# Optimization experiments

Measured on AMD Instinct MI355X. Metric: run time of the kernel, lower is better.

The kernel has to match this reference:

```python
import jax, jax.numpy as jnp
import numpy as np

B, S, D = 2, 2048, 1024
H, DH, DL = 16, 64, 512
E, DFF, K = 8, 2048, 2
EPS = 1e-5


def setup_inputs() -> dict:
    key = jax.random.key(0)
    ks = jax.random.split(key, 10)
    std = 0.02
    inp = {
        'x': jax.random.normal(ks[0], (B, S, D), jnp.float32),
        'mask': jnp.tril(jnp.ones((S, S), dtype=bool))[None, None],  # causal (1,1,S,S)
        'ln1_scale': jnp.ones((D,), jnp.float32),
        'ln1_bias': jnp.zeros((D,), jnp.float32),
        'Wq': jax.random.normal(ks[1], (D, H * DH), jnp.float32) * std,
        'Wdkv': jax.random.normal(ks[2], (D, DL), jnp.float32) * std,
        'Wukv': jax.random.normal(ks[3], (DL, H * DH), jnp.float32) * std,
        'Wo': jax.random.normal(ks[4], (H * DH, D), jnp.float32) * std,
        'ln2_scale': jnp.ones((D,), jnp.float32),
        'ln2_bias': jnp.zeros((D,), jnp.float32),
        'Wgate': jax.random.normal(ks[5], (D, E), jnp.float32) * std,
        'bgate': jnp.zeros((E,), jnp.float32),
        'We1': jax.random.normal(ks[6], (E, D, DFF), jnp.float32) * std,
        'be1': jnp.zeros((E, DFF), jnp.float32),
        'We2': jax.random.normal(ks[7], (E, DFF, D), jnp.float32) * std,
        'be2': jnp.zeros((E, D), jnp.float32),
    }
    return inp


def _layernorm(x, g, b):
    m = jnp.mean(x, axis=-1, keepdims=True)
    v = jnp.mean(jnp.square(x - m), axis=-1, keepdims=True)
    return (x - m) * jax.lax.rsqrt(v + EPS) * g + b


def reference(x, mask, ln1_scale, ln1_bias, Wq, Wdkv, Wukv, Wo,
              ln2_scale, ln2_bias, Wgate, bgate, We1, be1, We2, be2):
    b, s, d = x.shape
    # --- MLA attention ---
    h = _layernorm(x, ln1_scale, ln1_bias)
    q = (h @ Wq).reshape(b, s, H, DH)
    kv = ((h @ Wdkv) @ Wukv).reshape(b, s, H, DH)  # k == v == kv
    scores = jnp.einsum('bqhd,bkhd->bhqk', q, kv) / (DH ** 0.5)
    scores = jnp.where(mask, scores, -jnp.inf)
    probs = jax.nn.softmax(scores, axis=-1)
    attn = jnp.einsum('bhqk,bkhd->bqhd', probs, kv).reshape(b, s, H * DH)
    x = x + attn @ Wo
    # --- MoE ---
    h2 = _layernorm(x, ln2_scale, ln2_bias)
    xf = h2.reshape(-1, d)                     # (T, D)
    T = xf.shape[0]
    logits = xf @ Wgate + bgate                # (T, E)
    w, sel = jax.lax.top_k(logits, K)          # (T, K)
    w = jax.nn.softmax(w, axis=-1)
    # scatter top-k weights into dense (T, E) combine weights
    wfull = jnp.zeros((T, E), xf.dtype).at[jnp.arange(T)[:, None], sel].add(w)
    hid = jax.nn.gelu(jnp.einsum('td,edf->etf', xf, We1) + be1[:, None, :],
                      approximate=False)
    oute = jnp.einsum('etf,efd->etd', hid, We2) + be2[:, None, :]
    moe = jnp.einsum('te,etd->td', wfull, oute)
    return x + moe.reshape(b, s, d)
```

## Files before the change

### kernel.cpp

```cpp
#include <hip/hip_runtime.h>

#define EPS_LN 1e-5f

typedef __attribute__((ext_vector_type(4))) float f32x4;
typedef __attribute__((ext_vector_type(8))) __bf16 bf16x8;
typedef __attribute__((ext_vector_type(2))) unsigned int u32x2;
typedef unsigned int u32;
typedef unsigned short u16;

__device__ __forceinline__ u16 f2b(float f) {
  unsigned int u = __builtin_bit_cast(unsigned int, f);
  unsigned int r = (u + 0x7FFFu + ((u >> 16) & 1u)) >> 16;
  return (u16)r;
}
__device__ __forceinline__ float b2f(u16 s) {
  unsigned int u = ((unsigned int)s) << 16;
  return __builtin_bit_cast(float, u);
}
__device__ __forceinline__ void splitf(float v, u16& h, u16& l) {
  h = f2b(v); l = f2b(v - b2f(h));
}
__device__ __forceinline__ float gelu_exact(float v) {
  return 0.5f * v * (1.0f + erff(v * 0.70710678118654752440f));
}
__device__ __forceinline__ void gload16(const void* g, void* l) {
  __builtin_amdgcn_global_load_lds((const __attribute__((address_space(1))) u32*)g,
                                   (__attribute__((address_space(3))) u32*)l, 16, 0, 0);
}
__device__ __forceinline__ void pv_mfma(f32x4& o, u32x2 a, u32x2 b) {
  asm("s_nop 1\n\tv_mfma_f32_16x16x16_bf16 %0, %1, %2, %0" : "+v"(o) : "v"(a), "v"(b));
}
__device__ __forceinline__ int fsw(int row, int sc) {
  return row * 64 + ((((sc >> 3) ^ (row & 7))) << 3) + (sc & 7);
}

__global__ __launch_bounds__(256) void k_transpose_bf16(
    const float* __restrict__ src, u16* __restrict__ dst, int K, int N)
{
  __shared__ u16 t[64][65];
  long base = (long)blockIdx.z * (long)K * (long)N;
  const float* s = src + base;
  u16* d = dst + base;
  int n0 = blockIdx.x * 64, k0 = blockIdx.y * 64;
  int c = threadIdx.x & 63, r = threadIdx.x >> 6;
#pragma unroll
  for (int i = 0; i < 16; i++) {
    int k = r * 16 + i;
    t[c][k] = f2b(s[(long)(k0 + k) * N + n0 + c]);
  }
  __syncthreads();
#pragma unroll
  for (int i = 0; i < 16; i++) {
    int n = r * 16 + i;
    d[(long)(n0 + n) * K + k0 + c] = t[n][c];
  }
}

__global__ __launch_bounds__(256) void k_split_transpose(
    const float* __restrict__ src, u16* __restrict__ dh,
    u16* __restrict__ dl, int K, int N)
{
  __shared__ float t[64][65];
  int n0 = blockIdx.x * 64, k0 = blockIdx.y * 64;
  int c = threadIdx.x & 63, r4 = threadIdx.x >> 6;
#pragma unroll
  for (int i = 0; i < 16; i++) {
    int k = r4 * 16 + i;
    t[c][k] = src[(long)(k0 + k) * N + n0 + c];
  }
  __syncthreads();
#pragma unroll
  for (int i = 0; i < 16; i++) {
    int n = r4 * 16 + i;
    float v = t[n][c];
    u16 h = f2b(v);
    dh[(long)(n0 + n) * K + k0 + c] = h;
    dl[(long)(n0 + n) * K + k0 + c] = f2b(v - b2f(h));
  }
}

__global__ __launch_bounds__(256) void k_transpose_kv(
    const u16* __restrict__ inh, const u16* __restrict__ inl,
    u16* __restrict__ outh, u16* __restrict__ outl)
{
  __shared__ u16 th[64][65];
  __shared__ u16 tl[64][65];
  int bh = blockIdx.y, s0 = blockIdx.x * 64;
  int b = bh >> 4, h = bh & 15;
  int c = threadIdx.x & 63, r = threadIdx.x >> 6;
  long ibase = ((long)b * 2048 + s0) * 1024 + h * 64;
  long obase = (long)bh * 64 * 2048 + s0;
#pragma unroll
  for (int i = 0; i < 16; i++) {
    int k = r * 16 + i;
    th[c][k] = inh[ibase + (long)k * 1024 + c];
    tl[c][k] = inl[ibase + (long)k * 1024 + c];
  }
  __syncthreads();
#pragma unroll
  for (int i = 0; i < 16; i++) {
    int n = r * 16 + i;
    outh[obase + (long)n * 2048 + c] = th[n][c];
    outl[obase + (long)n * 2048 + c] = tl[n][c];
  }
}

template<int MODE>
__global__ __launch_bounds__(256) void k_layernorm(
    const float* __restrict__ x, const float* __restrict__ g,
    const float* __restrict__ b, u16* __restrict__ o1, u16* __restrict__ o2)
{
  int row = blockIdx.x, tid = threadIdx.x;
  const float* xr = x + (long)row * 1024;
  float4 v = *(const float4*)&xr[tid * 4];
  float s = v.x + v.y + v.z + v.w;
  float sq = v.x * v.x + v.y * v.y + v.z * v.z + v.w * v.w;
#pragma unroll
  for (int o = 32; o; o >>= 1) { s += __shfl_down(s, o); sq += __shfl_down(sq, o); }
  __shared__ float red[8];
  int wave = tid >> 6, lane = tid & 63;
  if (lane == 0) { red[wave] = s; red[4 + wave] = sq; }
  __syncthreads();
  s  = red[0] + red[1] + red[2] + red[3];
  sq = red[4] + red[5] + red[6] + red[7];
  float mean = s * (1.0f / 1024.0f);
  float var  = sq * (1.0f / 1024.0f) - mean * mean;
  float rs = rsqrtf(var + EPS_LN);
  float4 gg = *(const float4*)&g[tid * 4];
  float4 bb = *(const float4*)&b[tid * 4];
  float ov[4];
  ov[0] = (v.x - mean) * rs * gg.x + bb.x;
  ov[1] = (v.y - mean) * rs * gg.y + bb.y;
  ov[2] = (v.z - mean) * rs * gg.z + bb.z;
  ov[3] = (v.w - mean) * rs * gg.w + bb.w;
  if (MODE == 1) {
    ushort4 o4; o4.x = f2b(ov[0]); o4.y = f2b(ov[1]); o4.z = f2b(ov[2]); o4.w = f2b(ov[3]);
    *(ushort4*)&o1[(long)row * 1024 + tid * 4] = o4;
  } else {
    ushort4 hh, ll;
    splitf(ov[0], hh.x, ll.x); splitf(ov[1], hh.y, ll.y);
    splitf(ov[2], hh.z, ll.z); splitf(ov[3], hh.w, ll.w);
    *(ushort4*)&o1[(long)row * 1024 + tid * 4] = hh;
    *(ushort4*)&o2[(long)row * 1024 + tid * 4] = ll;
  }
}

template<int EPI>
__global__ __launch_bounds__(256) void k_gemm_bf3(
    const u16* __restrict__ Ah, const u16* __restrict__ Al,
    const u16* __restrict__ Bh, const u16* __restrict__ Bl,
    float* __restrict__ Cf, u16* __restrict__ Ch, u16* __restrict__ Cl,
    const float* __restrict__ aux, int M, int N, int K)
{
  int nwg = gridDim.x, cpx = nwg >> 3;
  int bid = blockIdx.x;
  int wg = (bid & 7) * cpx + (bid >> 3);
  int mm = M >> 7;
  int mb = wg % mm, nb = wg / mm;
  long m0 = (long)mb * 128, n0 = (long)nb * 128;
  __shared__ __align__(16) u16 sAh[2][4096], sAl[2][4096];
  __shared__ __align__(16) u16 sBh[2][4096], sBl[2][4096];
  int tid = threadIdx.x, lane = tid & 63, w = tid >> 6;
  int wr = w >> 1, wc = w & 1, l15 = lane & 15, l4 = lane >> 4;
  int r16 = lane >> 2, c8 = (lane & 3) * 8;
  long a0 = (m0 + w * 32 + r16) * (long)K + c8;
  long a1 = a0 + 16L * K;
  long b0 = (n0 + w * 32 + r16) * (long)K + c8;
  long b1 = b0 + 16L * K;
  int d0 = (w * 32) * 32, d1 = (w * 32 + 16) * 32;

  f32x4 acc[4][4];
  f32x4 zz = {0.0f, 0.0f, 0.0f, 0.0f};
#pragma unroll
  for (int i = 0; i < 4; i++)
#pragma unroll
    for (int j = 0; j < 4; j++) acc[i][j] = zz;

  gload16(&Ah[a0], &sAh[0][d0]); gload16(&Ah[a1], &sAh[0][d1]);
  gload16(&Al[a0], &sAl[0][d0]); gload16(&Al[a1], &sAl[0][d1]);
  gload16(&Bh[b0], &sBh[0][d0]); gload16(&Bh[b1], &sBh[0][d1]);
  gload16(&Bl[b0], &sBl[0][d0]); gload16(&Bl[b1], &sBl[0][d1]);
  __syncthreads();
  int cur = 0;
  for (int k0 = 0; k0 < K; k0 += 32) {
    int nxt = cur ^ 1;
    if (k0 + 32 < K) {
      long o = k0 + 32;
      gload16(&Ah[a0 + o], &sAh[nxt][d0]); gload16(&Ah[a1 + o], &sAh[nxt][d1]);
      gload16(&Al[a0 + o], &sAl[nxt][d0]); gload16(&Al[a1 + o], &sAl[nxt][d1]);
      gload16(&Bh[b0 + o], &sBh[nxt][d0]); gload16(&Bh[b1 + o], &sBh[nxt][d1]);
      gload16(&Bl[b0 + o], &sBl[nxt][d0]); gload16(&Bl[b1 + o], &sBl[nxt][d1]);
    }
    bf16x8 ah[4], al[4], bh[4], bl[4];
#pragma unroll
    for (int mi = 0; mi < 4; mi++) {
      int off = (wr * 64 + mi * 16 + l15) * 32 + l4 * 8;
      ah[mi] = *(const bf16x8*)&sAh[cur][off];
      al[mi] = *(const bf16x8*)&sAl[cur][off];
    }
#pragma unroll
    for (int ni = 0; ni < 4; ni++) {
      int off = (wc * 64 + ni * 16 + l15) * 32 + l4 * 8;
      bh[ni] = *(const bf16x8*)&sBh[cur][off];
      bl[ni] = *(const bf16x8*)&sBl[cur][off];
    }
#pragma unroll
    for (int mi = 0; mi < 4; mi++)
#pragma unroll
      for (int ni = 0; ni < 4; ni++) {
        acc[mi][ni] = __builtin_amdgcn_mfma_f32_16x16x32_bf16(ah[mi], bh[ni], acc[mi][ni], 0, 0, 0);
        acc[mi][ni] = __builtin_amdgcn_mfma_f32_16x16x32_bf16(ah[mi], bl[ni], acc[mi][ni], 0, 0, 0);
        acc[mi][ni] = __builtin_amdgcn_mfma_f32_16x16x32_bf16(al[mi], bh[ni], acc[mi][ni], 0, 0, 0);
      }
    __syncthreads();
    cur = nxt;
  }
#pragma unroll
  for (int mi = 0; mi < 4; mi++) {
#pragma unroll
    for (int j = 0; j < 4; j++) {
      long row = m0 + wr * 64 + mi * 16 + l4 * 4 + j;
#pragma unroll
      for (int ni = 0; ni < 4; ni++) {
        long col = n0 + wc * 64 + ni * 16 + l15;
        long idx = row * N + col;
        float vv = acc[mi][ni][j];
        if (EPI == 2) {
          u16 hh_, ll_; splitf(vv, hh_, ll_);
          Ch[idx] = hh_; Cl[idx] = ll_;
        } else {
          if (EPI == 1) vv += aux[idx];
          Cf[idx] = vv;
        }
      }
    }
  }
}

__global__ __launch_bounds__(256) void k_flash_v3(
    const u16* __restrict__ Qh, const u16* __restrict__ Ql,
    const u16* __restrict__ Kh, const u16* __restrict__ Kl,
    const u16* __restrict__ Th, const u16* __restrict__ Tl,
    u16* __restrict__ Oh, u16* __restrict__ Ol)
{
  int qb = (int)gridDim.y - 1 - (int)blockIdx.y;
  int bh = blockIdx.x;
  int q0 = qb * 64;
  int tid = threadIdx.x, lane = tid & 63, w = tid >> 6;
  int l15 = lane & 15, l4 = lane >> 4;
  __shared__ __align__(16) u16 Qsh[4096], Qsl[4096];
  __shared__ __align__(16) u16 Ksh[2][4096], Ksl[2][4096];
  __shared__ __align__(16) u16 Tsh[2][4096], Tsl[2][4096];
  long rowb = (long)(bh >> 4) * 2048;
  int  colo = (bh & 15) * 64;
  long tbase = (long)bh * 64 * 2048;
  int r8 = lane >> 3;
  int c8s = ((lane & 7) ^ r8) * 8;

#pragma unroll
  for (int k = 0; k < 2; k++) {
    int rr = w * 16 + k * 8;
    long src = (rowb + q0 + rr + r8) * 1024 + colo + c8s;
    gload16(&Qh[src], &Qsh[rr * 64]);
    gload16(&Ql[src], &Qsl[rr * 64]);
  }
#pragma unroll
  for (int k = 0; k < 2; k++) {
    int rr = w * 16 + k * 8;
    long srcK = (rowb + rr + r8) * 1024 + colo + c8s;
    long srcT = tbase + (long)(rr + r8) * 2048 + c8s;
    gload16(&Kh[srcK], &Ksh[0][rr * 64]);
    gload16(&Kl[srcK], &Ksl[0][rr * 64]);
    gload16(&Th[srcT], &Tsh[0][rr * 64]);
    gload16(&Tl[srcT], &Tsl[0][rr * 64]);
  }
  __syncthreads();

  float m = -1e30f, lsum = 0.0f;
  f32x4 o[4];
  f32x4 zz = {0.0f, 0.0f, 0.0f, 0.0f};
#pragma unroll
  for (int nb = 0; nb < 4; nb++) o[nb] = zz;
  int cur = 0;

  for (int kt = 0; kt <= qb; kt++) {
    int k0 = kt * 64;
    if (kt < qb) {
      int kn = k0 + 64, nxt = cur ^ 1;
#pragma unroll
      for (int k = 0; k < 2; k++) {
        int rr = w * 16 + k * 8;
        long srcK = (rowb + kn + rr + r8) * 1024 + colo + c8s;
        long srcT = tbase + (long)(rr + r8) * 2048 + kn + c8s;
        gload16(&Kh[srcK], &Ksh[nxt][rr * 64]);
        gload16(&Kl[srcK], &Ksl[nxt][rr * 64]);
        gload16(&Th[srcT], &Tsh[nxt][rr * 64]);
        gload16(&Tl[srcT], &Tsl[nxt][rr * 64]);
      }
    }
    f32x4 sT[4];
#pragma unroll
    for (int mi = 0; mi < 4; mi++) sT[mi] = zz;
#pragma unroll
    for (int ds = 0; ds < 2; ds++) {
      int qoff = fsw(w * 16 + l15, ds * 32 + l4 * 8);
      bf16x8 qh = *(const bf16x8*)&Qsh[qoff];
      bf16x8 ql = *(const bf16x8*)&Qsl[qoff];
#pragma unroll
      for (int mi = 0; mi < 4; mi++) {
        int koff = fsw(mi * 16 + l15, ds * 32 + l4 * 8);
        bf16x8 kh = *(const bf16x8*)&Ksh[cur][koff];
        bf16x8 kl = *(const bf16x8*)&Ksl[cur][koff];
        sT[mi] = __builtin_amdgcn_mfma_f32_16x16x32_bf16(kh, qh, sT[mi], 0, 0, 0);
        sT[mi] = __builtin_amdgcn_mfma_f32_16x16x32_bf16(kh, ql, sT[mi], 0, 0, 0);
        sT[mi] = __builtin_amdgcn_mfma_f32_16x16x32_bf16(kl, qh, sT[mi], 0, 0, 0);
      }
    }
    bool diag = (kt == qb);
    int qg = q0 + w * 16 + l15;
    float p[4][4];
    float tm = -1e30f;
#pragma unroll
    for (int mi = 0; mi < 4; mi++)
#pragma unroll
      for (int r = 0; r < 4; r++) {
        float v = sT[mi][r] * 0.125f;
        if (diag && (k0 + mi * 16 + l4 * 4 + r > qg)) v = -1e30f;
        p[mi][r] = v; tm = fmaxf(tm, v);
      }
    tm = fmaxf(tm, __shfl_xor(tm, 16));
    tm = fmaxf(tm, __shfl_xor(tm, 32));
    float mn = fmaxf(m, tm);
    float corr = __expf(m - mn);
    m = mn;
    float rs = 0.0f;
#pragma unroll
    for (int mi = 0; mi < 4; mi++)
#pragma unroll
      for (int r = 0; r < 4; r++) {
        float pv = __expf(p[mi][r] - mn);
        p[mi][r] = pv; rs += pv;
      }
    rs += __shfl_xor(rs, 16);
    rs += __shfl_xor(rs, 32);
    lsum = lsum * corr + rs;
    float corrO[4];
#pragma unroll
    for (int r = 0; r < 4; r++) corrO[r] = __shfl(corr, l4 * 4 + r);
#pragma unroll
    for (int nb = 0; nb < 4; nb++)
#pragma unroll
      for (int r = 0; r < 4; r++) o[nb][r] *= corrO[r];
    u32x2 pah[4], pal[4];
#pragma unroll
    for (int mi = 0; mi < 4; mi++) {
      u16 h[4], l[4];
#pragma unroll
      for (int r = 0; r < 4; r++) splitf(p[mi][r], h[r], l[r]);
      pah[mi][0] = (u32)h[0] | ((u32)h[1] << 16);
      pah[mi][1] = (u32)h[2] | ((u32)h[3] << 16);
      pal[mi][0] = (u32)l[0] | ((u32)l[1] << 16);
      pal[mi][1] = (u32)l[2] | ((u32)l[3] << 16);
    }
#pragma unroll
    for (int nb = 0; nb < 4; nb++) {
#pragma unroll
      for (int mi = 0; mi < 4; mi++) {
        int toff = fsw(nb * 16 + l15, mi * 16 + l4 * 4);
        u32x2 vh = *(const u32x2*)&Tsh[cur][toff];
        u32x2 vl = *(const u32x2*)&Tsl[cur][toff];
        pv_mfma(o[nb], pah[mi], vh);
        pv_mfma(o[nb], pah[mi], vl);
        pv_mfma(o[nb], pal[mi], vh);
      }
    }
    __syncthreads();
    cur ^= 1;
  }
  __builtin_amdgcn_sched_barrier(0);
  asm volatile("s_nop 7\n\ts_nop 7" ::: "memory");
  __builtin_amdgcn_sched_barrier(0);
  float inv[4];
#pragma unroll
  for (int r = 0; r < 4; r++) inv[r] = 1.0f / __shfl(lsum, l4 * 4 + r);
#pragma unroll
  for (int nb = 0; nb < 4; nb++)
#pragma unroll
    for (int r = 0; r < 4; r++) {
      long idx = (rowb + q0 + w * 16 + l4 * 4 + r) * 1024 + colo + nb * 16 + l15;
      u16 hh_, ll_; splitf(o[nb][r] * inv[r], hh_, ll_);
      Oh[idx] = hh_; Ol[idx] = ll_;
    }
}

__global__ __launch_bounds__(256) void k_gate(
    const float* __restrict__ x1, const float* __restrict__ g2, const float* __restrict__ b2,
    const float* __restrict__ Wg, const float* __restrict__ bg,
    int* __restrict__ sel, float* __restrict__ wts)
{
  int t = blockIdx.x * 4 + (threadIdx.x >> 6);
  int lane = threadIdx.x & 63;
  const float* xr = x1 + (long)t * 1024;
  float v[16], s = 0.0f, sq = 0.0f;
#pragma unroll
  for (int i = 0; i < 16; i++) { v[i] = xr[lane + 64 * i]; s += v[i]; sq += v[i] * v[i]; }
#pragma unroll
  for (int o = 32; o; o >>= 1) { s += __shfl_xor(s, o); sq += __shfl_xor(sq, o); }
  float mean = s * (1.0f / 1024.0f);
  float var = sq * (1.0f / 1024.0f) - mean * mean;
  float rs = rsqrtf(var + EPS_LN);
  float acc[8];
#pragma unroll
  for (int e = 0; e < 8; e++) acc[e] = 0.0f;
#pragma unroll
  for (int i = 0; i < 16; i++) {
    int d = lane + 64 * i;
    float hh = (v[i] - mean) * rs * g2[d] + b2[d];
    float4 w0 = *(const float4*)&Wg[d * 8];
    float4 w1 = *(const float4*)&Wg[d * 8 + 4];
    acc[0] += hh * w0.x; acc[1] += hh * w0.y; acc[2] += hh * w0.z; acc[3] += hh * w0.w;
    acc[4] += hh * w1.x; acc[5] += hh * w1.y; acc[6] += hh * w1.z; acc[7] += hh * w1.w;
  }
#pragma unroll
  for (int o = 32; o; o >>= 1)
#pragma unroll
    for (int e = 0; e < 8; e++) acc[e] += __shfl_xor(acc[e], o);
  if (lane == 0) {
    float le[8];
#pragma unroll
    for (int e = 0; e < 8; e++) le[e] = acc[e] + bg[e];
    int i0 = 0;
    for (int e = 1; e < 8; e++) if (le[e] > le[i0]) i0 = e;
    int i1 = (i0 == 0) ? 1 : 0;
    for (int e = 0; e < 8; e++) if (e != i0 && le[e] > le[i1]) i1 = e;
    float w0 = 1.0f / (1.0f + __expf(le[i1] - le[i0]));
    sel[2 * t] = i0; sel[2 * t + 1] = i1;
    wts[2 * t] = w0; wts[2 * t + 1] = 1.0f - w0;
  }
}

__global__ __launch_bounds__(256) void k_count(const int* __restrict__ sel, int* __restrict__ cnt)
{
  int e = blockIdx.x, tid = threadIdx.x;
  int c = 0;
  for (int t = tid; t < 4096; t += 256)
    c += (sel[2 * t] == e) + (sel[2 * t + 1] == e);
#pragma unroll
  for (int o = 32; o; o >>= 1) c += __shfl_down(c, o);
  __shared__ int red[4];
  int wave = tid >> 6, lane = tid & 63;
  if (lane == 0) red[wave] = c;
  __syncthreads();
  if (tid == 0) cnt[e] = red[0] + red[1] + red[2] + red[3];
}

__global__ void k_offsets(const int* __restrict__ cnt, int* __restrict__ offs)
{
  if (threadIdx.x == 0) {
    int a = 0; offs[0] = 0;
    for (int e = 0; e < 8; e++) { a += cnt[e]; offs[e + 1] = a; }
  }
}

__global__ __launch_bounds__(256) void k_scatter(
    const int* __restrict__ sel, const int* __restrict__ offs,
    int* __restrict__ tlist, int* __restrict__ slot_of)
{
  int e = blockIdx.x, tid = threadIdx.x;
  int lane = tid & 63, wave = tid >> 6;
  __shared__ int wsum[4];
  int base = offs[e];
  for (int t0 = 0; t0 < 4096; t0 += 256) {
    int t = t0 + tid;
    int s0 = sel[2 * t], s1 = sel[2 * t + 1];
    bool p = (s0 == e) || (s1 == e);
    int k = (s0 == e) ? 0 : 1;
    unsigned long long mb = __ballot(p);
    int rank = __popcll(mb & ((1ull << lane) - 1ull));
    if (lane == 0) wsum[wave] = __popcll(mb);
    __syncthreads();
    int wbase = 0;
    for (int w = 0; w < wave; w++) wbase += wsum[w];
    if (p) { int idx = base + wbase + rank; tlist[idx] = t; slot_of[2 * t + k] = idx; }
    base += wsum[0] + wsum[1] + wsum[2] + wsum[3];
    __syncthreads();
  }
}

template<int EPI>
__global__ __launch_bounds__(256) void k_gemm_moe(
    const u16* __restrict__ A, const u16* __restrict__ Bt,
    void* __restrict__ Cout, const float* __restrict__ bias,
    const int* __restrict__ tlist, const int* __restrict__ offs,
    int N, int K, long strideB, int strideBias)
{
  int e = blockIdx.x & 7, slot = blockIdx.x >> 3;
  int r0 = offs[e], r1 = offs[e + 1];
  int rows = r1 - r0;
  if (rows <= 0) return;
  int nn = N >> 7;
  int ntiles = ((rows + 127) >> 7) * nn;
  const u16* B = Bt + (long)e * strideB;
  const float* bvec = bias + (long)e * strideBias;
  __shared__ __align__(16) u16 lA[2][128 * 64];
  __shared__ __align__(16) u16 lB[2][128 * 64];
  int tid = threadIdx.x, lane = tid & 63, w = tid >> 6;
  int wr = w >> 1, wc = w & 1;
  int l15 = lane & 15, l4 = lane >> 4;
  int lr8 = lane >> 3;
  int csrc = ((lane & 7) ^ lr8) * 8;
  int nt = K >> 6;

  for (int t = slot; t < ntiles; t += 256) {
    int rbk = t / nn, nb = t - rbk * nn;
    int m0 = r0 + rbk * 128;
    long n0 = (long)nb * 128;
    u32 asrc[4], bsrc[4];
#pragma unroll
    for (int r = 0; r < 4; r++) {
      int row = w * 32 + r * 8 + lr8;
      int g = m0 + row; if (g > r1 - 1) g = r1 - 1;
      int ar = (EPI == 2) ? tlist[g] : g;
      asrc[r] = (u32)ar * (u32)K + csrc;
      bsrc[r] = (u32)(n0 + row) * (u32)K + csrc;
    }
    f32x4 acc[4][4];
    f32x4 zz = {0.0f, 0.0f, 0.0f, 0.0f};
#pragma unroll
    for (int i = 0; i < 4; i++)
#pragma unroll
      for (int j = 0; j < 4; j++) acc[i][j] = zz;

#define STAGE_MOE(buf, k0_) do { u32 o_ = (k0_); \
    _Pragma("unroll") \
    for (int r = 0; r < 4; r++) { \
      gload16(&A[asrc[r] + o_], &lA[buf][(w * 32 + r * 8) * 64]); \
      gload16(&B[bsrc[r] + o_], &lB[buf][(w * 32 + r * 8) * 64]); \
    } } while (0)

    STAGE_MOE(0, 0);
    __syncthreads();
    int cur = 0;
    for (int s = 0; s < nt; s++) {
      if (s + 1 < nt) STAGE_MOE(cur ^ 1, (u32)(s + 1) * 64);
#pragma unroll
      for (int ks = 0; ks < 2; ks++) {
        bf16x8 af[4], bq[4];
#pragma unroll
        for (int mi = 0; mi < 4; mi++) {
          int row = wr * 64 + mi * 16 + l15;
          af[mi] = *(const bf16x8*)&lA[cur][row * 64 + (((ks * 4 + l4) ^ (l15 & 7)) * 8)];
        }
#pragma unroll
        for (int ni = 0; ni < 4; ni++) {
          int row = wc * 64 + ni * 16 + l15;
          bq[ni] = *(const bf16x8*)&lB[cur][row * 64 + (((ks * 4 + l4) ^ (l15 & 7)) * 8)];
        }
#pragma unroll
        for (int mi = 0; mi < 4; mi++)
#pragma unroll
          for (int ni = 0; ni < 4; ni++)
            acc[mi][ni] = __builtin_amdgcn_mfma_f32_16x16x32_bf16(af[mi], bq[ni], acc[mi][ni], 0, 0, 0);
      }
      __syncthreads();
      cur ^= 1;
    }
#undef STAGE_MOE
#pragma unroll
    for (int mi = 0; mi < 4; mi++) {
#pragma unroll
      for (int j = 0; j < 4; j++) {
        int row = m0 + wr * 64 + mi * 16 + l4 * 4 + j;
        if (row < r1) {
#pragma unroll
          for (int ni = 0; ni < 4; ni++) {
            long col = n0 + wc * 64 + ni * 16 + l15;
            float vv = acc[mi][ni][j] + bvec[col];
            if (EPI == 2) {
              ((u16*)Cout)[(long)row * N + col] = f2b(gelu_exact(vv));
            } else {
              ((float*)Cout)[(long)row * N + col] = vv;
            }
          }
        }
      }
    }
  }
}

__global__ __launch_bounds__(256) void k_combine(
    const float* __restrict__ x1, const float* __restrict__ oute,
    const int* __restrict__ slot_of, const float* __restrict__ wts,
    float* __restrict__ out)
{
  int t = blockIdx.x;
  int c = threadIdx.x * 4;
  int s0 = slot_of[2 * t], s1 = slot_of[2 * t + 1];
  float w0 = wts[2 * t], w1 = wts[2 * t + 1];
  float4 a  = *(const float4*)&x1[(long)t * 1024 + c];
  float4 e0 = *(const float4*)&oute[(long)s0 * 1024 + c];
  float4 e1 = *(const float4*)&oute[(long)s1 * 1024 + c];
  float4 r;
  r.x = a.x + w0 * e0.x + w1 * e1.x;
  r.y = a.y + w0 * e0.y + w1 * e1.y;
  r.z = a.z + w0 * e0.z + w1 * e1.z;
  r.w = a.w + w0 * e0.w + w1 * e1.w;
  *(float4*)&out[(long)t * 1024 + c] = r;
}

extern "C" void kernel_launch(void* const* d_in, const int* in_sizes, int n_in,
                              void* d_out, int out_size, void* d_ws, size_t ws_size,
                              hipStream_t stream)
{
  const float* x    = (const float*)d_in[0];
  const float* ln1s = (const float*)d_in[2];
  const float* ln1b = (const float*)d_in[3];
  const float* Wq   = (const float*)d_in[4];
  const float* Wdkv = (const float*)d_in[5];
  const float* Wukv = (const float*)d_in[6];
  const float* Wo   = (const float*)d_in[7];
  const float* ln2s = (const float*)d_in[8];
  const float* ln2b = (const float*)d_in[9];
  const float* Wg   = (const float*)d_in[10];
  const float* bg   = (const float*)d_in[11];
  const float* We1  = (const float*)d_in[12];
  const float* be1  = (const float*)d_in[13];
  const float* We2  = (const float*)d_in[14];
  const float* be2  = (const float*)d_in[15];
  float* out = (float*)d_out;

  char* wp = (char*)d_ws;
  auto take = [&](size_t nbytes) -> void* {
    char* r = wp; wp += (nbytes + 255) & ~(size_t)255; return (void*)r;
  };
  u16* We1t = (u16*)take(8L * 2048 * 1024 * 2);
  u16* We2t = (u16*)take(8L * 1024 * 2048 * 2);
  u16* hh   = (u16*)take(4096L * 1024 * 2);
  u16* hl   = (u16*)take(4096L * 1024 * 2);
  u16* qh   = (u16*)take(4096L * 1024 * 2);
  u16* ql   = (u16*)take(4096L * 1024 * 2);
  u16* kvh  = (u16*)take(4096L * 1024 * 2);
  u16* kvl  = (u16*)take(4096L * 1024 * 2);
  u16* kvTh = (u16*)take(4096L * 1024 * 2);
  u16* kvTl = (u16*)take(4096L * 1024 * 2);
  u16* cbh  = (u16*)take(4096L * 512 * 2);
  u16* cbl  = (u16*)take(4096L * 512 * 2);
  float* x1 = (float*)take(4096L * 1024 * 4);
  u16* hid  = (u16*)take(8192L * 2048 * 2);
  int*   sel   = (int*)take(8192 * 4);
  float* wts   = (float*)take(8192 * 4);
  int*   cnt   = (int*)take(64);
  int*   offs  = (int*)take(64);
  int*   tlist = (int*)take(8192 * 4);
  int*   slot  = (int*)take(8192 * 4);
  u16* attn_h = hh;
  u16* attn_l = hl;
  u16* h2bf   = cbh;
  float* oute = (float*)qh;
  u16* Wqh   = hid;
  u16* Wql   = Wqh   + 1024L * 1024;
  u16* Wdkvh = Wql   + 1024L * 1024;
  u16* Wdkvl = Wdkvh + 512L * 1024;
  u16* Wukvh = Wdkvl + 512L * 1024;
  u16* Wukvl = Wukvh + 1024L * 512;
  u16* Woh   = Wukvl + 1024L * 512;
  u16* Wol   = Woh   + 1024L * 1024;
  if ((size_t)(wp - (char*)d_ws) > ws_size) return;

  dim3 b256(256);
  k_transpose_bf16<<<dim3(32, 16, 8), b256, 0, stream>>>(We1, We1t, 1024, 2048);
  k_transpose_bf16<<<dim3(16, 32, 8), b256, 0, stream>>>(We2, We2t, 2048, 1024);
  k_split_transpose<<<dim3(16, 16), b256, 0, stream>>>(Wq,   Wqh,   Wql,   1024, 1024);
  k_split_transpose<<<dim3(8, 16),  b256, 0, stream>>>(Wdkv, Wdkvh, Wdkvl, 1024, 512);
  k_split_transpose<<<dim3(16, 8),  b256, 0, stream>>>(Wukv, Wukvh, Wukvl, 512, 1024);
  k_split_transpose<<<dim3(16, 16), b256, 0, stream>>>(Wo,   Woh,   Wol,   1024, 1024);
  k_layernorm<2><<<dim3(4096), b256, 0, stream>>>(x, ln1s, ln1b, hh, hl);
  k_gemm_bf3<2><<<dim3(256), b256, 0, stream>>>(hh, hl, Wqh, Wql, nullptr, qh, ql,
                                                nullptr, 4096, 1024, 1024);
  k_gemm_bf3<2><<<dim3(128), b256, 0, stream>>>(hh, hl, Wdkvh, Wdkvl, nullptr, cbh, cbl,
                                                nullptr, 4096, 512, 1024);
  k_gemm_bf3<2><<<dim3(256), b256, 0, stream>>>(cbh, cbl, Wukvh, Wukvl, nullptr, kvh, kvl,
                                                nullptr, 4096, 1024, 512);
  k_transpose_kv<<<dim3(32, 32), b256, 0, stream>>>(kvh, kvl, kvTh, kvTl);
  k_flash_v3<<<dim3(32, 32), b256, 0, stream>>>(qh, ql, kvh, kvl, kvTh, kvTl, attn_h, attn_l);
  k_gemm_bf3<1><<<dim3(256), b256, 0, stream>>>(attn_h, attn_l, Woh, Wol, x1, nullptr, nullptr,
                                                x, 4096, 1024, 1024);
  k_layernorm<1><<<dim3(4096), b256, 0, stream>>>(x1, ln2s, ln2b, h2bf, nullptr);
  k_gate<<<dim3(1024), b256, 0, stream>>>(x1, ln2s, ln2b, Wg, bg, sel, wts);
  k_count<<<dim3(8), b256, 0, stream>>>(sel, cnt);
  k_offsets<<<dim3(1), dim3(64), 0, stream>>>(cnt, offs);
  k_scatter<<<dim3(8), b256, 0, stream>>>(sel, offs, tlist, slot);
  k_gemm_moe<2><<<dim3(2048), b256, 0, stream>>>(h2bf, We1t, hid, be1, tlist, offs,
                                                 2048, 1024, 2048L * 1024, 2048);
  k_gemm_moe<3><<<dim3(2048), b256, 0, stream>>>(hid, We2t, oute, be2, tlist, offs,
                                                 1024, 2048, 1024L * 2048, 1024);
  k_combine<<<dim3(4096), b256, 0, stream>>>(x1, oute, slot, wts, out);
}
```

Baseline: 575.4 us.

## Enlarge MoE GEMM tiles to 256x256 with 512-thread blocks and BK=32

Reworks the expert GEMM kernel to compute 256x256 output tiles per block using 8 waves (2x4), with a K-step of 32 instead of 64 and a new LDS swizzle. Each wave now holds an 8x4 accumulator array and reuses B fragments across 8 A rows, raising arithmetic intensity per LDS/global load. Grid shrinks to 512 blocks with 64 slots per expert. Risks: higher register pressure, fewer tiles per expert (worse load balance and occupancy), and more sync per K since the K-step halves.

```diff
diff --git a/kernel.cpp b/kernel.cpp
--- a/kernel.cpp
+++ b/kernel.cpp
@@ -488,7 +488,7 @@
 }
 
 template<int EPI>
-__global__ __launch_bounds__(256) void k_gemm_moe(
+__global__ __launch_bounds__(512, 1) void k_gemm_moe(
     const u16* __restrict__ A, const u16* __restrict__ Bt,
     void* __restrict__ Cout, const float* __restrict__ bias,
     const int* __restrict__ tlist, const int* __restrict__ offs,
@@ -498,79 +498,72 @@
   int r0 = offs[e], r1 = offs[e + 1];
   int rows = r1 - r0;
   if (rows <= 0) return;
-  int nn = N >> 7;
-  int ntiles = ((rows + 127) >> 7) * nn;
+  int nn = N >> 8;
+  int ntiles = ((rows + 255) >> 8) * nn;
   const u16* B = Bt + (long)e * strideB;
   const float* bvec = bias + (long)e * strideBias;
-  __shared__ __align__(16) u16 lA[2][128 * 64];
-  __shared__ __align__(16) u16 lB[2][128 * 64];
+  __shared__ __align__(16) u16 lA[2][256 * 32];
+  __shared__ __align__(16) u16 lB[2][256 * 32];
   int tid = threadIdx.x, lane = tid & 63, w = tid >> 6;
-  int wr = w >> 1, wc = w & 1;
+  int wr = w >> 2, wc = w & 3;
   int l15 = lane & 15, l4 = lane >> 4;
-  int lr8 = lane >> 3;
-  int csrc = ((lane & 7) ^ lr8) * 8;
-  int nt = K >> 6;
-
-  for (int t = slot; t < ntiles; t += 256) {
+  int q = lane >> 2;
+  int csrc = ((lane & 3) ^ ((lane >> 3) & 3)) * 8;
+  int rsw = (l15 >> 1) & 3;
+  int nt = K >> 5;
+
+  for (int t = slot; t < ntiles; t += 64) {
     int rbk = t / nn, nb = t - rbk * nn;
-    int m0 = r0 + rbk * 128;
-    long n0 = (long)nb * 128;
-    u32 asrc[4], bsrc[4];
-#pragma unroll
-    for (int r = 0; r < 4; r++) {
-      int row = w * 32 + r * 8 + lr8;
+    int m0 = r0 + rbk * 256;
+    long n0 = (long)nb * 256;
+    u32 asrc[2], bsrc[2];
+#pragma unroll
+    for (int rr = 0; rr < 2; rr++) {
+      int row = w * 32 + rr * 16 + q;
       int g = m0 + row; if (g > r1 - 1) g = r1 - 1;
       int ar = (EPI == 2) ? tlist[g] : g;
-      asrc[r] = (u32)ar * (u32)K + csrc;
-      bsrc[r] = (u32)(n0 + row) * (u32)K + csrc;
-    }
-    f32x4 acc[4][4];
+      asrc[rr] = (u32)ar * (u32)K + csrc;
+      bsrc[rr] = (u32)(n0 + row) * (u32)K + csrc;
+    }
+    f32x4 acc[8][4];
     f32x4 zz = {0.0f, 0.0f, 0.0f, 0.0f};
 #pragma unroll
-    for (int i = 0; i < 4; i++)
+    for (int i = 0; i < 8; i++)
 #pragma unroll
       for (int j = 0; j < 4; j++) acc[i][j] = zz;
 
-#define STAGE_MOE(buf, k0_) do { u32 o_ = (k0_); \
+#define STAGE_MOE(buf, ko) do { \
     _Pragma("unroll") \
-    for (int r = 0; r < 4; r++) { \
-      gload16(&A[asrc[r] + o_], &lA[buf][(w * 32 + r * 8) * 64]); \
-      gload16(&B[bsrc[r] + o_], &lB[buf][(w * 32 + r * 8) * 64]); \
+    for (int rr = 0; rr < 2; rr++) { \
+      gload16(&A[asrc[rr] + (ko)], &lA[buf][(w * 32 + rr * 16) * 32]); \
+      gload16(&B[bsrc[rr] + (ko)], &lB[buf][(w * 32 + rr * 16) * 32]); \
     } } while (0)
 
     STAGE_MOE(0, 0);
     __syncthreads();
     int cur = 0;
     for (int s = 0; s < nt; s++) {
-      if (s + 1 < nt) STAGE_MOE(cur ^ 1, (u32)(s + 1) * 64);
-#pragma unroll
-      for (int ks = 0; ks < 2; ks++) {
-        bf16x8 af[4], bq[4];
-#pragma unroll
-        for (int mi = 0; mi < 4; mi++) {
-          int row = wr * 64 + mi * 16 + l15;
-          af[mi] = *(const bf16x8*)&lA[cur][row * 64 + (((ks * 4 + l4) ^ (l15 & 7)) * 8)];
-        }
-#pragma unroll
-        for (int ni = 0; ni < 4; ni++) {
-          int row = wc * 64 + ni * 16 + l15;
-          bq[ni] = *(const bf16x8*)&lB[cur][row * 64 + (((ks * 4 + l4) ^ (l15 & 7)) * 8)];
-        }
-#pragma unroll
-        for (int mi = 0; mi < 4; mi++)
-#pragma unroll
-          for (int ni = 0; ni < 4; ni++)
-            acc[mi][ni] = __builtin_amdgcn_mfma_f32_16x16x32_bf16(af[mi], bq[ni], acc[mi][ni], 0, 0, 0);
+      if (s + 1 < nt) STAGE_MOE(cur ^ 1, (u32)(s + 1) * 32);
+      bf16x8 bfr[4];
+#pragma unroll
+      for (int ni = 0; ni < 4; ni++)
+        bfr[ni] = *(const bf16x8*)&lB[cur][(wc * 64 + ni * 16 + l15) * 32 + ((l4 ^ rsw) * 8)];
+#pragma unroll
+      for (int mi = 0; mi < 8; mi++) {
+        bf16x8 afr = *(const bf16x8*)&lA[cur][(wr * 128 + mi * 16 + l15) * 32 + ((l4 ^ rsw) * 8)];
+#pragma unroll
+        for (int ni = 0; ni < 4; ni++)
+          acc[mi][ni] = __builtin_amdgcn_mfma_f32_16x16x32_bf16(afr, bfr[ni], acc[mi][ni], 0, 0, 0);
       }
       __syncthreads();
       cur ^= 1;
     }
 #undef STAGE_MOE
 #pragma unroll
-    for (int mi = 0; mi < 4; mi++) {
+    for (int mi = 0; mi < 8; mi++) {
 #pragma unroll
       for (int j = 0; j < 4; j++) {
-        int row = m0 + wr * 64 + mi * 16 + l4 * 4 + j;
+        int row = m0 + wr * 128 + mi * 16 + l4 * 4 + j;
         if (row < r1) {
 #pragma unroll
           for (int ni = 0; ni < 4; ni++) {
@@ -667,7 +660,7 @@
   u16* Wol   = Woh   + 1024L * 1024;
   if ((size_t)(wp - (char*)d_ws) > ws_size) return;
 
-  dim3 b256(256);
+  dim3 b256(256), b512(512);
   k_transpose_bf16<<<dim3(32, 16, 8), b256, 0, stream>>>(We1, We1t, 1024, 2048);
   k_transpose_bf16<<<dim3(16, 32, 8), b256, 0, stream>>>(We2, We2t, 2048, 1024);
   k_split_transpose<<<dim3(16, 16), b256, 0, stream>>>(Wq,   Wqh,   Wql,   1024, 1024);
@@ -690,9 +683,9 @@
   k_count<<<dim3(8), b256, 0, stream>>>(sel, cnt);
   k_offsets<<<dim3(1), dim3(64), 0, stream>>>(cnt, offs);
   k_scatter<<<dim3(8), b256, 0, stream>>>(sel, offs, tlist, slot);
-  k_gemm_moe<2><<<dim3(2048), b256, 0, stream>>>(h2bf, We1t, hid, be1, tlist, offs,
-                                                 2048, 1024, 2048L * 1024, 2048);
-  k_gemm_moe<3><<<dim3(2048), b256, 0, stream>>>(hid, We2t, oute, be2, tlist, offs,
-                                                 1024, 2048, 1024L * 2048, 1024);
+  k_gemm_moe<2><<<dim3(512), b512, 0, stream>>>(h2bf, We1t, hid, be1, tlist, offs,
+                                                2048, 1024, 2048L * 1024, 2048);
+  k_gemm_moe<3><<<dim3(512), b512, 0, stream>>>(hid, We2t, oute, be2, tlist, offs,
+                                                1024, 2048, 1024L * 2048, 1024);
   k_combine<<<dim3(4096), b256, 0, stream>>>(x1, oute, slot, wts, out);
 }
```

After: 652.7 us. 13.4% more time.

## Split-K the attention projection GEMMs with separate reduction kernels

Applied to the files above, without the earlier changes.

The bf16x3 projection GEMM now splits K in two across paired workgroups, doubling the grid to fill more compute units. Each half writes fp32 partials to a scratch buffer aliased onto the We2 transposed buffer. New reduce kernels sum the halves and apply the hi/lo split or the residual add. The expert weight transposes move after the attention stage so the scratch can reuse that memory. The cost is extra fp32 partial traffic to global memory plus four additional kernel launches.

```diff
diff --git a/kernel.cpp b/kernel.cpp
--- a/kernel.cpp
+++ b/kernel.cpp
@@ -145,27 +145,28 @@
   }
 }
 
-template<int EPI>
 __global__ __launch_bounds__(256) void k_gemm_bf3(
     const u16* __restrict__ Ah, const u16* __restrict__ Al,
     const u16* __restrict__ Bh, const u16* __restrict__ Bl,
-    float* __restrict__ Cf, u16* __restrict__ Ch, u16* __restrict__ Cl,
-    const float* __restrict__ aux, int M, int N, int K)
-{
-  int nwg = gridDim.x, cpx = nwg >> 3;
-  int bid = blockIdx.x;
+    float* __restrict__ P, int M, int N, int K)
+{
+  int split = blockIdx.x & 1;
+  int bid = blockIdx.x >> 1;
+  int nwg = gridDim.x >> 1, cpx = nwg >> 3;
   int wg = (bid & 7) * cpx + (bid >> 3);
   int mm = M >> 7;
   int mb = wg % mm, nb = wg / mm;
   long m0 = (long)mb * 128, n0 = (long)nb * 128;
+  int K2 = K >> 1;
+  int kbase = split * K2;
   __shared__ __align__(16) u16 sAh[2][4096], sAl[2][4096];
   __shared__ __align__(16) u16 sBh[2][4096], sBl[2][4096];
   int tid = threadIdx.x, lane = tid & 63, w = tid >> 6;
   int wr = w >> 1, wc = w & 1, l15 = lane & 15, l4 = lane >> 4;
   int r16 = lane >> 2, c8 = (lane & 3) * 8;
-  long a0 = (m0 + w * 32 + r16) * (long)K + c8;
+  long a0 = (m0 + w * 32 + r16) * (long)K + kbase + c8;
   long a1 = a0 + 16L * K;
-  long b0 = (n0 + w * 32 + r16) * (long)K + c8;
+  long b0 = (n0 + w * 32 + r16) * (long)K + kbase + c8;
   long b1 = b0 + 16L * K;
   int d0 = (w * 32) * 32, d1 = (w * 32 + 16) * 32;
 
@@ -182,9 +183,9 @@
   gload16(&Bl[b0], &sBl[0][d0]); gload16(&Bl[b1], &sBl[0][d1]);
   __syncthreads();
   int cur = 0;
-  for (int k0 = 0; k0 < K; k0 += 32) {
+  for (int k0 = 0; k0 < K2; k0 += 32) {
     int nxt = cur ^ 1;
-    if (k0 + 32 < K) {
+    if (k0 + 32 < K2) {
       long o = k0 + 32;
       gload16(&Ah[a0 + o], &sAh[nxt][d0]); gload16(&Ah[a1 + o], &sAh[nxt][d1]);
       gload16(&Al[a0 + o], &sAl[nxt][d0]); gload16(&Al[a1 + o], &sAl[nxt][d1]);
@@ -215,6 +216,7 @@
     __syncthreads();
     cur = nxt;
   }
+  long base = (long)split * M * N;
 #pragma unroll
   for (int mi = 0; mi < 4; mi++) {
 #pragma unroll
@@ -223,18 +225,35 @@
 #pragma unroll
       for (int ni = 0; ni < 4; ni++) {
         long col = n0 + wc * 64 + ni * 16 + l15;
-        long idx = row * N + col;
-        float vv = acc[mi][ni][j];
-        if (EPI == 2) {
-          u16 hh_, ll_; splitf(vv, hh_, ll_);
-          Ch[idx] = hh_; Cl[idx] = ll_;
-        } else {
-          if (EPI == 1) vv += aux[idx];
-          Cf[idx] = vv;
-        }
-      }
-    }
-  }
+        P[base + row * N + col] = acc[mi][ni][j];
+      }
+    }
+  }
+}
+
+__global__ __launch_bounds__(256) void k_red_split(
+    const float* __restrict__ P, u16* __restrict__ Ch, u16* __restrict__ Cl, long MN)
+{
+  long i = ((long)blockIdx.x * 256 + threadIdx.x) * 4;
+  float4 a = *(const float4*)&P[i];
+  float4 b = *(const float4*)&P[MN + i];
+  ushort4 h, l;
+  splitf(a.x + b.x, h.x, l.x); splitf(a.y + b.y, h.y, l.y);
+  splitf(a.z + b.z, h.z, l.z); splitf(a.w + b.w, h.w, l.w);
+  *(ushort4*)&Ch[i] = h;
+  *(ushort4*)&Cl[i] = l;
+}
+
+__global__ __launch_bounds__(256) void k_red_resid(
+    const float* __restrict__ P, const float* __restrict__ x,
+    float* __restrict__ out, long MN)
+{
+  long i = ((long)blockIdx.x * 256 + threadIdx.x) * 4;
+  float4 a = *(const float4*)&P[i];
+  float4 b = *(const float4*)&P[MN + i];
+  float4 xv = *(const float4*)&x[i];
+  float4 r = {a.x + b.x + xv.x, a.y + b.y + xv.y, a.z + b.z + xv.z, a.w + b.w + xv.w};
+  *(float4*)&out[i] = r;
 }
 
 __global__ __launch_bounds__(256) void k_flash_v3(
@@ -657,6 +676,7 @@
   u16* attn_l = hl;
   u16* h2bf   = cbh;
   float* oute = (float*)qh;
+  float* Pk   = (float*)We2t;
   u16* Wqh   = hid;
   u16* Wql   = Wqh   + 1024L * 1024;
   u16* Wdkvh = Wql   + 1024L * 1024;
@@ -668,28 +688,28 @@
   if ((size_t)(wp - (char*)d_ws) > ws_size) return;
 
   dim3 b256(256);
-  k_transpose_bf16<<<dim3(32, 16, 8), b256, 0, stream>>>(We1, We1t, 1024, 2048);
-  k_transpose_bf16<<<dim3(16, 32, 8), b256, 0, stream>>>(We2, We2t, 2048, 1024);
   k_split_transpose<<<dim3(16, 16), b256, 0, stream>>>(Wq,   Wqh,   Wql,   1024, 1024);
   k_split_transpose<<<dim3(8, 16),  b256, 0, stream>>>(Wdkv, Wdkvh, Wdkvl, 1024, 512);
   k_split_transpose<<<dim3(16, 8),  b256, 0, stream>>>(Wukv, Wukvh, Wukvl, 512, 1024);
   k_split_transpose<<<dim3(16, 16), b256, 0, stream>>>(Wo,   Woh,   Wol,   1024, 1024);
   k_layernorm<2><<<dim3(4096), b256, 0, stream>>>(x, ln1s, ln1b, hh, hl);
-  k_gemm_bf3<2><<<dim3(256), b256, 0, stream>>>(hh, hl, Wqh, Wql, nullptr, qh, ql,
-                                                nullptr, 4096, 1024, 1024);
-  k_gemm_bf3<2><<<dim3(128), b256, 0, stream>>>(hh, hl, Wdkvh, Wdkvl, nullptr, cbh, cbl,
-                                                nullptr, 4096, 512, 1024);
-  k_gemm_bf3<2><<<dim3(256), b256, 0, stream>>>(cbh, cbl, Wukvh, Wukvl, nullptr, kvh, kvl,
-                                                nullptr, 4096, 1024, 512);
+  k_gemm_bf3<<<dim3(512), b256, 0, stream>>>(hh, hl, Wqh, Wql, Pk, 4096, 1024, 1024);
+  k_red_split<<<dim3(4096), b256, 0, stream>>>(Pk, qh, ql, 4096L * 1024);
+  k_gemm_bf3<<<dim3(256), b256, 0, stream>>>(hh, hl, Wdkvh, Wdkvl, Pk, 4096, 512, 1024);
+  k_red_split<<<dim3(2048), b256, 0, stream>>>(Pk, cbh, cbl, 4096L * 512);
+  k_gemm_bf3<<<dim3(512), b256, 0, stream>>>(cbh, cbl, Wukvh, Wukvl, Pk, 4096, 1024, 512);
+  k_red_split<<<dim3(4096), b256, 0, stream>>>(Pk, kvh, kvl, 4096L * 1024);
   k_transpose_kv<<<dim3(32, 32), b256, 0, stream>>>(kvh, kvl, kvTh, kvTl);
   k_flash_v3<<<dim3(32, 32), b256, 0, stream>>>(qh, ql, kvh, kvl, kvTh, kvTl, attn_h, attn_l);
-  k_gemm_bf3<1><<<dim3(256), b256, 0, stream>>>(attn_h, attn_l, Woh, Wol, x1, nullptr, nullptr,
-                                                x, 4096, 1024, 1024);
+  k_gemm_bf3<<<dim3(512), b256, 0, stream>>>(attn_h, attn_l, Woh, Wol, Pk, 4096, 1024, 1024);
+  k_red_resid<<<dim3(4096), b256, 0, stream>>>(Pk, x, x1, 4096L * 1024);
   k_layernorm<1><<<dim3(4096), b256, 0, stream>>>(x1, ln2s, ln2b, h2bf, nullptr);
   k_gate<<<dim3(1024), b256, 0, stream>>>(x1, ln2s, ln2b, Wg, bg, sel, wts);
   k_count<<<dim3(8), b256, 0, stream>>>(sel, cnt);
   k_offsets<<<dim3(1), dim3(64), 0, stream>>>(cnt, offs);
   k_scatter<<<dim3(8), b256, 0, stream>>>(sel, offs, tlist, slot);
+  k_transpose_bf16<<<dim3(32, 16, 8), b256, 0, stream>>>(We1, We1t, 1024, 2048);
+  k_transpose_bf16<<<dim3(16, 32, 8), b256, 0, stream>>>(We2, We2t, 2048, 1024);
   k_gemm_moe<2><<<dim3(2048), b256, 0, stream>>>(h2bf, We1t, hid, be1, tlist, offs,
                                                  2048, 1024, 2048L * 1024, 2048);
   k_gemm_moe<3><<<dim3(2048), b256, 0, stream>>>(hid, We2t, oute, be2, tlist, offs,
```

After: 502.1 us. 12.7% less time.
